# Optimization experiments

Measured on AMD Instinct MI355X. Metric: run time of the kernel, lower is better.

The kernel has to match this reference:

```python
import jax, jax.numpy as jnp
import numpy as np

B, T1, T2, D, H = 16, 512, 64, 768, 12
E = D // H  # head dim


def _proj(x, W, b):
    # x: [B,T,D], W: [6,D,D], b: [6,D] -> [6,B,H,T,E], scaled by E**-0.25 (applied to q,k,v alike, per source)
    t = x.shape[1]
    p = jnp.einsum('btd,kdf->kbtf', x, W) + b[:, None, None, :]
    p = p.reshape(6, B, t, H, E).transpose(0, 1, 3, 2, 4)
    return p * (E ** -0.25)


def setup_inputs() -> dict:
    key = jax.random.key(0)
    ks = jax.random.split(key, 12)
    s = 0.02
    return {
        'feats': jax.random.normal(ks[0], (B, T1, D), jnp.float32),
        'inps': jax.random.normal(ks[1], (B, T2, D), jnp.float32),
        'att_mask': jax.random.randint(ks[2], (B, 1, 1, T1 + T2), 0, 2).astype(bool),
        'W_f': s * jax.random.normal(ks[3], (6, D, D), jnp.float32),
        'b_f': s * jax.random.normal(ks[4], (6, D), jnp.float32),
        'W_i': s * jax.random.normal(ks[5], (6, D, D), jnp.float32),
        'b_i': s * jax.random.normal(ks[6], (6, D), jnp.float32),
        'Wu_v': s * jax.random.normal(ks[7], (D, D), jnp.float32),
        'bu_v': s * jax.random.normal(ks[8], (D,), jnp.float32),
        'Wu_l': s * jax.random.normal(ks[9], (D, D), jnp.float32),
        'bu_l': s * jax.random.normal(ks[10], (D,), jnp.float32),
    }


def reference(feats, inps, att_mask, W_f, b_f, W_i, b_i, Wu_v, bu_v, Wu_l, bu_l):
    NEG = jnp.float32(-1e9)
    # projections from feats: [keys_v_v, queries_v_v, values_v_v, queries_l_v, keys_v_l, values_v_l]
    k_vv, q_vv, v_vv, q_lv, k_vl, v_vl = _proj(feats, W_f, b_f)
    # projections from inps: [keys_l_v, values_l_v, queries_v_l, queries_l_l, keys_l_l, values_l_l]
    k_lv, v_lv, q_vl, q_ll, k_ll, v_ll = _proj(inps, W_i, b_i)

    # visual stream: two distinct queries over the two key blocks, joint softmax over t1+t2
    dot_vv = jnp.einsum('bhqe,bhke->bhqk', q_vv, k_vv)   # [B,H,T1,T1]
    dot_lv = jnp.einsum('bhqe,bhke->bhqk', q_lv, k_lv)   # [B,H,T1,T2]
    att_v = jnp.concatenate([dot_vv, dot_lv], axis=-1)    # [B,H,T1,T1+T2]
    att_v = jax.nn.softmax(jnp.where(att_mask, NEG, att_v), axis=-1)
    vals_v = jnp.concatenate([v_vv, v_lv], axis=2)        # [B,H,T1+T2,E]
    out_v = jnp.einsum('bhqk,bhke->bhqe', att_v, vals_v)
    out_v = out_v.transpose(0, 2, 1, 3).reshape(B, T1, D)
    out_v = out_v @ Wu_v + bu_v

    # language stream
    dot_vl = jnp.einsum('bhqe,bhke->bhqk', q_vl, k_vl)    # [B,H,T2,T1]
    dot_ll = jnp.einsum('bhqe,bhke->bhqk', q_ll, k_ll)    # [B,H,T2,T2]
    att_l = jnp.concatenate([dot_vl, dot_ll], axis=-1)    # [B,H,T2,T1+T2]
    att_l = jax.nn.softmax(jnp.where(att_mask, NEG, att_l), axis=-1)
    vals_l = jnp.concatenate([v_vl, v_ll], axis=2)        # [B,H,T1+T2,E]
    out_l = jnp.einsum('bhqk,bhke->bhqe', att_l, vals_l)
    out_l = out_l.transpose(0, 2, 1, 3).reshape(B, T2, D)
    out_l = out_l @ Wu_l + bu_l

    return (out_v, out_l)
```

## Files before the change

kernel.cpp:

```cpp
#include <hip/hip_runtime.h>
#include <stdint.h>

#define BB 16
#define T1C 512
#define T2C 64
#define DC 768
#define HC 12
#define EC 64
#define SC 576
#define QSCALE 0.35355339059327379f

typedef __attribute__((ext_vector_type(8))) short bf16x8;
typedef __attribute__((ext_vector_type(4))) float f32x4;

__device__ __forceinline__ uint16_t f2b(float f) {
    union { float f; uint32_t i; } v; v.f = f;
    return (uint16_t)((v.i + 0x7fffu + ((v.i >> 16) & 1u)) >> 16);
}
__device__ __forceinline__ uint16_t f2bfast(float f) {
    union { float f; uint32_t i; } v; v.f = f;
    return (uint16_t)((v.i + 0x8000u) >> 16);
}
__device__ __forceinline__ uint32_t pk2(float a, float b) {
    return (uint32_t)f2b(a) | ((uint32_t)f2b(b) << 16);
}

__device__ __forceinline__ void gll16(const void* g, void* l) {
    __builtin_amdgcn_global_load_lds(
        (const __attribute__((address_space(1))) uint32_t*)(uintptr_t)g,
        (__attribute__((address_space(3))) uint32_t*)(uintptr_t)l, 16, 0, 0);
}

__global__ void detect(const uint32_t* __restrict__ mw, int* __restrict__ flags) {
    __shared__ int aW, aB, aL;
    if (threadIdx.x == 0) { aW = 0; aB = 0; aL = 0; }
    __syncthreads();
    int lW = 0, lB = 0, lL = 0;
    for (int i = threadIdx.x; i < 2304; i += 256) {
        uint32_t w = mw[i];
        if (w > 1u) lW = 1;
        if (((w) & 0xffu) > 1u || ((w >> 8) & 0xffu) > 1u ||
            ((w >> 16) & 0xffu) > 1u || ((w >> 24) & 0xffu) > 1u) lB = 1;
        if ((w & 0xffffu) > 1u) lL = 1;
    }
    if (lW) atomicOr(&aW, 1);
    if (lB) atomicOr(&aB, 1);
    if (lL) atomicOr(&aL, 1);
    __syncthreads();
    if (threadIdx.x == 0)
        flags[0] = (!aW) ? 0 : ((!aB) ? 1 : (aL ? 2 : 0));
}

__global__ __launch_bounds__(256) void wtrans(
    const float* __restrict__ Wf, const float* __restrict__ Wi,
    const float* __restrict__ Wuv, const float* __restrict__ Wul,
    uint16_t* __restrict__ Wt)
{
    __shared__ float tile[32][33];
    const int z = blockIdx.z;
    const float* src = (z < 6)  ? Wf + (size_t)z * DC * DC
                     : (z < 12) ? Wi + (size_t)(z - 6) * DC * DC
                     : (z == 12 ? Wuv : Wul);
    uint16_t* dst = Wt + (size_t)z * DC * DC;
    const int tx = threadIdx.x & 31, ty = threadIdx.x >> 5;
    const int k0 = blockIdx.x * 32, f0 = blockIdx.y * 32;
#pragma unroll
    for (int r = 0; r < 4; r++)
        tile[ty + r * 8][tx] = src[(size_t)(k0 + ty + r * 8) * DC + f0 + tx];
    __syncthreads();
#pragma unroll
    for (int r = 0; r < 4; r++)
        dst[(size_t)(f0 + ty + r * 8) * DC + k0 + tx] = f2b(tile[tx][ty + r * 8]);
}

__global__ __launch_bounds__(256) void xswz(
    const float* __restrict__ Xf, const float* __restrict__ Xi,
    uint16_t* __restrict__ Of, uint16_t* __restrict__ Oi)
{
    const int nf = BB * T1C * DC / 8;
    const int ni = BB * T2C * DC / 8;
    int t = blockIdx.x * 256 + threadIdx.x;
    const float* src; uint16_t* dst; int cc;
    if (t < nf) { src = Xf; dst = Of; cc = t; }
    else        { cc = t - nf; if (cc >= ni) return; src = Xi; dst = Oi; }
    int rlid = cc & 15;
    int t2 = cc >> 4;
    int qd = t2 & 3;
    int t3 = t2 >> 2;
    int kt = t3 % 24;
    int p  = t3 / 24;
    const float* sp = src + (size_t)(p * 16 + rlid) * DC + kt * 32 + qd * 8;
    float4 a = *(const float4*)sp;
    float4 b = *(const float4*)(sp + 4);
    uint4 o;
    o.x = pk2(a.x, a.y); o.y = pk2(a.z, a.w);
    o.z = pk2(b.x, b.y); o.w = pk2(b.z, b.w);
    *(uint4*)(dst + (size_t)cc * 8) = o;
}

#define BSTR 76

__global__ __launch_bounds__(256, 3) void gemm_proj_mfma(
    const uint16_t* __restrict__ Xsf, const uint16_t* __restrict__ Xsi,
    const uint16_t* __restrict__ Wt,
    const float* __restrict__ b_f, const float* __restrict__ b_i,
    uint16_t* __restrict__ Pf, uint16_t* __restrict__ Pi)
{
    __shared__ union {
        uint16_t B[128 * 32];
        uint16_t bounce[4][16 * BSTR];
    } sm;
    const int tid = threadIdx.x;
    const int w = tid >> 6, l = tid & 63;
    const bool isf = (blockIdx.x < 64);
    const int mx = isf ? blockIdx.x : blockIdx.x - 64;
    const int m0 = mx * 128;
    const int T  = isf ? T1C : T2C;
    const uint16_t* Xs = isf ? Xsf : Xsi;
    const float* bias  = isf ? b_f : b_i;
    uint16_t* P        = isf ? Pf : Pi;
    const int vmask    = isf ? 0x24 : 0x22;
    const int k6 = blockIdx.y / 6, nt = blockIdx.y % 6;
    const int n0 = nt * 128;
    const uint16_t* Bsrc = Wt + (size_t)((isf ? 0 : 6) + k6) * DC * DC;

    const int lid = l & 15, qd = l >> 4;
    const int wm = w >> 1, wn = w & 1;
    const int br = l >> 2, bk = (l & 3) * 8;
    const int p0 = mx * 8 + wm * 4;

    f32x4 acc[4][4] = {};

    for (int kt = 0; kt < DC / 32; ++kt) {
        __syncthreads();
#pragma unroll
        for (int n = 0; n < 2; ++n) {
            int c = w * 2 + n;
            gll16(Bsrc + (size_t)(n0 + c * 16 + br) * DC + kt * 32 + bk, &sm.B[c * 512]);
        }
        bf16x8 af[4];
#pragma unroll
        for (int i = 0; i < 4; i++)
            af[i] = *(const bf16x8*)(Xs + ((size_t)((p0 + i) * 24 + kt) * 64 + l) * 8);
        __syncthreads();
        bf16x8 bf[4];
#pragma unroll
        for (int j = 0; j < 4; j++)
            bf[j] = *(const bf16x8*)&sm.B[(wn * 64 + j * 16 + lid) * 32 + qd * 8];
#pragma unroll
        for (int i = 0; i < 4; i++)
#pragma unroll
            for (int j = 0; j < 4; j++)
                acc[i][j] = __builtin_amdgcn_mfma_f32_16x16x32_bf16(af[i], bf[j], acc[i][j], 0, 0, 0);
    }

    float bv[4];
#pragma unroll
    for (int j = 0; j < 4; j++)
        bv[j] = bias[k6 * DC + n0 + wn * 64 + j * 16 + lid];
    __syncthreads();

    uint16_t* reg = sm.bounce[w];
    const int mb = m0 + wm * 64;
    const int b = mb / T, tb = mb - b * T;
    const int h = nt * 2 + wn;
    const int rrow = l >> 2;
    const int rcol = (l & 3) * 16;

    if (!((vmask >> k6) & 1)) {
        uint16_t* dst0 = P + ((((size_t)k6 * BB + b) * HC + h) * T + tb + rrow) * EC + rcol;
#pragma unroll
        for (int p = 0; p < 4; p++) {
#pragma unroll
            for (int j = 0; j < 4; j++)
#pragma unroll
                for (int r = 0; r < 4; r++)
                    reg[(qd * 4 + r) * BSTR + j * 16 + lid] =
                        f2b((acc[p][j][r] + bv[j]) * QSCALE);
            uint4 d0 = *(const uint4*)&reg[rrow * BSTR + rcol];
            uint4 d1 = *(const uint4*)&reg[rrow * BSTR + rcol + 8];
            uint16_t* dst = dst0 + (size_t)p * 16 * EC;
            *(uint4*)dst = d0;
            *(uint4*)(dst + 8) = d1;
        }
    } else {
        uint16_t* dst0 = P + (size_t)k6 * BB * HC * T * EC
                           + (((size_t)b * HC + h) * EC + rrow) * T + tb + rcol;
#pragma unroll
        for (int p = 0; p < 4; p++) {
#pragma unroll
            for (int i = 0; i < 4; i++) {
                uint32_t w0 = pk2((acc[i][p][0] + bv[p]) * QSCALE,
                                  (acc[i][p][1] + bv[p]) * QSCALE);
                uint32_t w1 = pk2((acc[i][p][2] + bv[p]) * QSCALE,
                                  (acc[i][p][3] + bv[p]) * QSCALE);
                *(uint2*)&reg[lid * BSTR + i * 16 + qd * 4] = make_uint2(w0, w1);
            }
            uint4 d0 = *(const uint4*)&reg[rrow * BSTR + rcol];
            uint4 d1 = *(const uint4*)&reg[rrow * BSTR + rcol + 8];
            uint16_t* dst = dst0 + (size_t)p * 16 * T;
            *(uint4*)dst = d0;
            *(uint4*)(dst + 8) = d1;
        }
    }
}

__global__ __launch_bounds__(256, 3) void gemm_out_mfma(
    const uint16_t* __restrict__ Osv, const uint16_t* __restrict__ Osl,
    const uint16_t* __restrict__ Wt,
    const float* __restrict__ bu_v, const float* __restrict__ bu_l,
    float* __restrict__ out)
{
    __shared__ uint16_t Bs[128 * 32];
    const int tid = threadIdx.x;
    const int w = tid >> 6, l = tid & 63;
    const bool isv = (blockIdx.x < 64);
    const int mx = isv ? blockIdx.x : blockIdx.x - 64;
    const int m0 = mx * 128;
    const int rowoff = isv ? 0 : BB * T1C;
    const uint16_t* A = isv ? Osv : Osl;
    const uint16_t* Wtm = Wt + (size_t)(isv ? 12 : 13) * DC * DC;
    const float* bias = isv ? bu_v : bu_l;
    const int n0 = blockIdx.y * 128;
    const int lid = l & 15, qd = l >> 4;
    const int wm = w >> 1, wn = w & 1;
    const int br = l >> 2, bk = (l & 3) * 8;
    const int p0 = mx * 8 + wm * 4;

    f32x4 acc[4][4] = {};

    for (int kt = 0; kt < DC / 32; ++kt) {
        __syncthreads();
#pragma unroll
        for (int n = 0; n < 2; ++n) {
            int c = w * 2 + n;
            gll16(Wtm + (size_t)(n0 + c * 16 + br) * DC + kt * 32 + bk, &Bs[c * 512]);
        }
        bf16x8 af[4];
#pragma unroll
        for (int i = 0; i < 4; i++)
            af[i] = *(const bf16x8*)(A + ((size_t)((p0 + i) * 24 + kt) * 64 + l) * 8);
        __syncthreads();
        bf16x8 bf[4];
#pragma unroll
        for (int j = 0; j < 4; j++)
            bf[j] = *(const bf16x8*)&Bs[(wn * 64 + j * 16 + lid) * 32 + qd * 8];
#pragma unroll
        for (int i = 0; i < 4; i++)
#pragma unroll
            for (int j = 0; j < 4; j++)
                acc[i][j] = __builtin_amdgcn_mfma_f32_16x16x32_bf16(af[i], bf[j], acc[i][j], 0, 0, 0);
    }

    float bv[4];
#pragma unroll
    for (int j = 0; j < 4; j++)
        bv[j] = bias[n0 + wn * 64 + j * 16 + lid];
#pragma unroll
    for (int i = 0; i < 4; i++)
#pragma unroll
        for (int j = 0; j < 4; j++)
#pragma unroll
            for (int r = 0; r < 4; r++) {
                int m = m0 + wm * 64 + i * 16 + qd * 4 + r;
                int f = n0 + wn * 64 + j * 16 + lid;
                out[(size_t)(rowoff + m) * DC + f] = acc[i][j][r] + bv[j];
            }
}

__global__ __launch_bounds__(256, 3) void attn_mfma(
    const uint16_t* __restrict__ Pf,
    const uint16_t* __restrict__ Pi,
    const void* __restrict__ maskp,
    const int* __restrict__ flags,
    uint16_t* __restrict__ Osv,
    uint16_t* __restrict__ Osl)
{
    __shared__ uint16_t Klds[64 * 72];
    __shared__ uint16_t Vlds[64 * 72];
    __shared__ uint16_t Plds[4][16 * 72];
    __shared__ float    Ma[SC];
    __shared__ float    Lw[4][16];

    const int bh = blockIdx.x;
    const int tile = blockIdx.y;
    const int b = bh / HC, h = bh % HC;
    const int tid = threadIdx.x;
    const int w = tid >> 6, l = tid & 63;
    const int lid = l & 15, qd = l >> 4;

    const size_t SF = (size_t)BB * HC * T1C * EC;
    const size_t SI = (size_t)BB * HC * T2C * EC;

    const bool vis = (tile < 8);
    const uint16_t *Qa, *Qb, *K1, *K2, *V1, *V2;
    uint16_t* O; int Tq, q0;
    if (vis) { Qa = Pf + 1 * SF; Qb = Pf + 3 * SF; K1 = Pf;          K2 = Pi;
               V1 = Pf + 2 * SF; V2 = Pi + 1 * SI; O = Osv; Tq = T1C; q0 = tile * 64; }
    else     { Qa = Pi + 2 * SI; Qb = Pi + 3 * SI; K1 = Pf + 4 * SF; K2 = Pi + 4 * SI;
               V1 = Pf + 5 * SF; V2 = Pi + 5 * SI; O = Osl; Tq = T2C; q0 = 0; }

    {
        const int kind = flags[0];
        for (int i = tid; i < SC; i += 256) {
            int idx = b * SC + i;
            int mv;
            if (kind == 0)      mv = ((const uint32_t*)maskp)[idx] != 0u;
            else if (kind == 1) mv = ((const uint8_t*)maskp)[idx] != 0;
            else                mv = ((const uint16_t*)maskp)[idx] != 0;
            Ma[i] = mv ? -1e9f : 0.0f;
        }
    }

    const int q = q0 + w * 16 + lid;
    const uint16_t* Qrow  = Qa + ((size_t)bh * Tq + q) * EC;
    const uint16_t* Qrow2 = Qb + ((size_t)bh * Tq + q) * EC;
    bf16x8 qf0 = *(const bf16x8*)(Qrow + qd * 8);
    bf16x8 qf1 = *(const bf16x8*)(Qrow + 32 + qd * 8);
    bf16x8 qg0 = *(const bf16x8*)(Qrow2 + qd * 8);
    bf16x8 qg1 = *(const bf16x8*)(Qrow2 + 32 + qd * 8);

    f32x4 o[4];
#pragma unroll
    for (int ef = 0; ef < 4; ef++) { o[ef][0]=0.f; o[ef][1]=0.f; o[ef][2]=0.f; o[ef][3]=0.f; }
    float u[4] = {0.f, 0.f, 0.f, 0.f};

    const int skey = tid >> 2, se0 = (tid & 3) * 16;
    const int ve = tid >> 2,  vc = tid & 3;

    auto kptr = [&](int c) -> const uint16_t* {
        return (c < 8) ? K1 + ((size_t)bh * T1C + c * 64 + skey) * EC + se0
                       : K2 + ((size_t)bh * T2C + skey) * EC + se0;
    };
    auto vptr = [&](int c) -> const uint16_t* {
        return (c < 8) ? V1 + ((size_t)bh * EC + ve) * T1C + c * 64 + vc * 16
                       : V2 + ((size_t)bh * EC + ve) * T2C + vc * 16;
    };

    uint4 ka0 = *(const uint4*)kptr(0);
    uint4 ka1 = *(const uint4*)(kptr(0) + 8);
    uint4 va0 = *(const uint4*)vptr(0);
    uint4 va1 = *(const uint4*)(vptr(0) + 8);

#pragma unroll
    for (int c = 0; c < 9; ++c) {
        uint4 kb0, kb1, vb0, vb1;
        if (c < 8) {
            kb0 = *(const uint4*)kptr(c + 1);
            kb1 = *(const uint4*)(kptr(c + 1) + 8);
            vb0 = *(const uint4*)vptr(c + 1);
            vb1 = *(const uint4*)(vptr(c + 1) + 8);
        }
        __builtin_amdgcn_s_barrier();
        __builtin_amdgcn_sched_barrier(0);
        *(uint4*)&Klds[skey * 72 + se0]         = ka0;
        *(uint4*)&Klds[skey * 72 + se0 + 8]     = ka1;
        *(uint4*)&Vlds[ve * 72 + vc * 16]       = va0;
        *(uint4*)&Vlds[ve * 72 + vc * 16 + 8]   = va1;
        asm volatile("s_waitcnt lgkmcnt(0)" ::: "memory");
        __builtin_amdgcn_sched_barrier(0);
        __builtin_amdgcn_s_barrier();
        __builtin_amdgcn_sched_barrier(0);

        const int k0 = c * 64;
        const bf16x8 q_0 = (c < 8) ? qf0 : qg0;
        const bf16x8 q_1 = (c < 8) ? qf1 : qg1;
        f32x4 s[4];
#pragma unroll
        for (int sub = 0; sub < 4; sub++) {
            bf16x8 kf0 = *(const bf16x8*)&Klds[(sub * 16 + lid) * 72 + qd * 8];
            bf16x8 kf1 = *(const bf16x8*)&Klds[(sub * 16 + lid) * 72 + 32 + qd * 8];
            f32x4 z; z[0]=0.f; z[1]=0.f; z[2]=0.f; z[3]=0.f;
            z = __builtin_amdgcn_mfma_f32_16x16x32_bf16(q_0, kf0, z, 0, 0, 0);
            s[sub] = __builtin_amdgcn_mfma_f32_16x16x32_bf16(q_1, kf1, z, 0, 0, 0);
        }
#pragma unroll
        for (int sub = 0; sub < 4; sub++) {
            float mv = Ma[k0 + sub * 16 + lid];
#pragma unroll
            for (int r = 0; r < 4; r++) {
                float p = __expf(s[sub][r] + mv);
                u[r] += p;
                Plds[w][(qd * 4 + r) * 72 + sub * 16 + lid] = f2bfast(p);
            }
        }
#pragma unroll
        for (int half = 0; half < 2; half++) {
            bf16x8 pf = *(const bf16x8*)&Plds[w][lid * 72 + half * 32 + qd * 8];
#pragma unroll
            for (int ef = 0; ef < 4; ef++) {
                bf16x8 vf = *(const bf16x8*)&Vlds[(ef * 16 + lid) * 72 + half * 32 + qd * 8];
                o[ef] = __builtin_amdgcn_mfma_f32_16x16x32_bf16(vf, pf, o[ef], 0, 0, 0);
            }
        }
        if (c < 8) { ka0 = kb0; ka1 = kb1; va0 = vb0; va1 = vb1; }
    }

#pragma unroll
    for (int d = 1; d <= 8; d <<= 1)
#pragma unroll
        for (int r = 0; r < 4; r++)
            u[r] += __shfl_xor(u[r], d, 64);
    if (lid == 0) {
#pragma unroll
        for (int r = 0; r < 4; r++) Lw[w][qd * 4 + r] = u[r];
    }
    float rl = 1.f / Lw[w][lid];

    const size_t p = ((size_t)b * Tq + q0 + w * 16) >> 4;
#pragma unroll
    for (int ef = 0; ef < 4; ef++) {
        uint32_t w0 = pk2(o[ef][0] * rl, o[ef][1] * rl);
        uint32_t w1 = pk2(o[ef][2] * rl, o[ef][3] * rl);
        size_t chunk = ((p * 24 + h * 2 + (ef >> 1)) * 4 + (ef & 1) * 2 + (qd >> 1)) * 16 + lid;
        *(uint2*)(O + chunk * 8 + (qd & 1) * 4) = make_uint2(w0, w1);
    }
}

extern "C" void kernel_launch(void* const* d_in, const int* in_sizes, int n_in,
                              void* d_out, int out_size, void* d_ws, size_t ws_size,
                              hipStream_t stream)
{
    const float* feats = (const float*)d_in[0];
    const float* inps  = (const float*)d_in[1];
    const void*  maskp = d_in[2];
    const float* W_f   = (const float*)d_in[3];
    const float* b_f   = (const float*)d_in[4];
    const float* W_i   = (const float*)d_in[5];
    const float* b_i   = (const float*)d_in[6];
    const float* Wu_v  = (const float*)d_in[7];
    const float* bu_v  = (const float*)d_in[8];
    const float* Wu_l  = (const float*)d_in[9];
    const float* bu_l  = (const float*)d_in[10];

    const size_t MAT = (size_t)DC * DC;
    const size_t PF_E = 6ull * BB * HC * T1C * EC;
    const size_t PI_E = 6ull * BB * HC * T2C * EC;
    uint16_t* Wt  = (uint16_t*)d_ws;
    uint16_t* Osv = Wt;
    uint16_t* Osl = Wt + (size_t)BB * T1C * HC * EC;
    uint16_t* Pf  = Wt + 14 * MAT;
    uint16_t* Pi  = Pf + PF_E;
    int* flags    = (int*)(Pi + PI_E);

    uint16_t* Xsf = (uint16_t*)d_out;
    uint16_t* Xsi = Xsf + (size_t)BB * T1C * DC;

    detect<<<dim3(1), dim3(256), 0, stream>>>((const uint32_t*)maskp, flags);

    wtrans<<<dim3(24, 24, 14), dim3(256), 0, stream>>>(W_f, W_i, Wu_v, Wu_l, Wt);

    {
        int nchunks = (BB * T1C * DC + BB * T2C * DC) / 8;
        xswz<<<dim3((nchunks + 255) / 256), dim3(256), 0, stream>>>(feats, inps, Xsf, Xsi);
    }

    gemm_proj_mfma<<<dim3(72, 36), dim3(256), 0, stream>>>(
        Xsf, Xsi, Wt, b_f, b_i, Pf, Pi);

    attn_mfma<<<dim3(BB * HC, 9), dim3(256), 0, stream>>>(
        Pf, Pi, maskp, flags, Osv, Osl);

    gemm_out_mfma<<<dim3(72, 6), dim3(256), 0, stream>>>(
        Osv, Osl, Wt, bu_v, bu_l, (float*)d_out);
}
```

Baseline: 270.6 us.

## Double-buffer weight tiles in LDS with async prefetch in both GEMMs

Both the projection and output GEMM kernels now keep two LDS buffers for the weight tile. The next k-slice is loaded asynchronously into the spare buffer while the current one feeds the MFMAs, and explicit vmcnt waits and barriers replace the two __syncthreads per iteration. This is meant to hide global-to-LDS latency behind compute. Launch bounds rise from 3 to 4 blocks per CU, which tightens the register budget, and the LDS footprint doubles.

```diff
diff --git a/kernel.cpp b/kernel.cpp
--- a/kernel.cpp
+++ b/kernel.cpp
@@ -100,14 +100,14 @@
 
 #define BSTR 76
 
-__global__ __launch_bounds__(256, 3) void gemm_proj_mfma(
+__global__ __launch_bounds__(256, 4) void gemm_proj_mfma(
     const uint16_t* __restrict__ Xsf, const uint16_t* __restrict__ Xsi,
     const uint16_t* __restrict__ Wt,
     const float* __restrict__ b_f, const float* __restrict__ b_i,
     uint16_t* __restrict__ Pf, uint16_t* __restrict__ Pi)
 {
     __shared__ union {
-        uint16_t B[128 * 32];
+        uint16_t B[2][128 * 32];
         uint16_t bounce[4][16 * BSTR];
     } sm;
     const int tid = threadIdx.x;
@@ -128,25 +128,39 @@
     const int wm = w >> 1, wn = w & 1;
     const int br = l >> 2, bk = (l & 3) * 8;
     const int p0 = mx * 8 + wm * 4;
+    const int c0 = w * 2;
 
     f32x4 acc[4][4] = {};
 
+#pragma unroll
+    for (int n = 0; n < 2; ++n)
+        gll16(Bsrc + (size_t)(n0 + (c0 + n) * 16 + br) * DC + bk, &sm.B[0][(c0 + n) * 512]);
+
     for (int kt = 0; kt < DC / 32; ++kt) {
-        __syncthreads();
-#pragma unroll
-        for (int n = 0; n < 2; ++n) {
-            int c = w * 2 + n;
-            gll16(Bsrc + (size_t)(n0 + c * 16 + br) * DC + kt * 32 + bk, &sm.B[c * 512]);
-        }
+        uint16_t* Bcur = sm.B[kt & 1];
+        uint16_t* Bnxt = sm.B[(kt + 1) & 1];
         bf16x8 af[4];
 #pragma unroll
         for (int i = 0; i < 4; i++)
             af[i] = *(const bf16x8*)(Xs + ((size_t)((p0 + i) * 24 + kt) * 64 + l) * 8);
-        __syncthreads();
+        __builtin_amdgcn_s_barrier();
+        __builtin_amdgcn_sched_barrier(0);
+        if (kt < 23) {
+#pragma unroll
+            for (int n = 0; n < 2; ++n)
+                gll16(Bsrc + (size_t)(n0 + (c0 + n) * 16 + br) * DC + (kt + 1) * 32 + bk,
+                      &Bnxt[(c0 + n) * 512]);
+            asm volatile("s_waitcnt vmcnt(2)" ::: "memory");
+        } else {
+            asm volatile("s_waitcnt vmcnt(0)" ::: "memory");
+        }
+        __builtin_amdgcn_sched_barrier(0);
+        __builtin_amdgcn_s_barrier();
+        __builtin_amdgcn_sched_barrier(0);
         bf16x8 bf[4];
 #pragma unroll
         for (int j = 0; j < 4; j++)
-            bf[j] = *(const bf16x8*)&sm.B[(wn * 64 + j * 16 + lid) * 32 + qd * 8];
+            bf[j] = *(const bf16x8*)&Bcur[(wn * 64 + j * 16 + lid) * 32 + qd * 8];
 #pragma unroll
         for (int i = 0; i < 4; i++)
 #pragma unroll
@@ -205,13 +219,13 @@
     }
 }
 
-__global__ __launch_bounds__(256, 3) void gemm_out_mfma(
+__global__ __launch_bounds__(256, 4) void gemm_out_mfma(
     const uint16_t* __restrict__ Osv, const uint16_t* __restrict__ Osl,
     const uint16_t* __restrict__ Wt,
     const float* __restrict__ bu_v, const float* __restrict__ bu_l,
     float* __restrict__ out)
 {
-    __shared__ uint16_t Bs[128 * 32];
+    __shared__ uint16_t Bs[2][128 * 32];
     const int tid = threadIdx.x;
     const int w = tid >> 6, l = tid & 63;
     const bool isv = (blockIdx.x < 64);
@@ -226,25 +240,39 @@
     const int wm = w >> 1, wn = w & 1;
     const int br = l >> 2, bk = (l & 3) * 8;
     const int p0 = mx * 8 + wm * 4;
+    const int c0 = w * 2;
 
     f32x4 acc[4][4] = {};
 
+#pragma unroll
+    for (int n = 0; n < 2; ++n)
+        gll16(Wtm + (size_t)(n0 + (c0 + n) * 16 + br) * DC + bk, &Bs[0][(c0 + n) * 512]);
+
     for (int kt = 0; kt < DC / 32; ++kt) {
-        __syncthreads();
-#pragma unroll
-        for (int n = 0; n < 2; ++n) {
-            int c = w * 2 + n;
-            gll16(Wtm + (size_t)(n0 + c * 16 + br) * DC + kt * 32 + bk, &Bs[c * 512]);
-        }
+        uint16_t* Bcur = Bs[kt & 1];
+        uint16_t* Bnxt = Bs[(kt + 1) & 1];
         bf16x8 af[4];
 #pragma unroll
         for (int i = 0; i < 4; i++)
             af[i] = *(const bf16x8*)(A + ((size_t)((p0 + i) * 24 + kt) * 64 + l) * 8);
-        __syncthreads();
+        __builtin_amdgcn_s_barrier();
+        __builtin_amdgcn_sched_barrier(0);
+        if (kt < 23) {
+#pragma unroll
+            for (int n = 0; n < 2; ++n)
+                gll16(Wtm + (size_t)(n0 + (c0 + n) * 16 + br) * DC + (kt + 1) * 32 + bk,
+                      &Bnxt[(c0 + n) * 512]);
+            asm volatile("s_waitcnt vmcnt(2)" ::: "memory");
+        } else {
+            asm volatile("s_waitcnt vmcnt(0)" ::: "memory");
+        }
+        __builtin_amdgcn_sched_barrier(0);
+        __builtin_amdgcn_s_barrier();
+        __builtin_amdgcn_sched_barrier(0);
         bf16x8 bf[4];
 #pragma unroll
         for (int j = 0; j < 4; j++)
-            bf[j] = *(const bf16x8*)&Bs[(wn * 64 + j * 16 + lid) * 32 + qd * 8];
+            bf[j] = *(const bf16x8*)&Bcur[(wn * 64 + j * 16 + lid) * 32 + qd * 8];
 #pragma unroll
         for (int i = 0; i < 4; i++)
 #pragma unroll
```

Measured after the change: 264.4 us. 2.3% less time.
